# Performance work log

Hardware: AMD Instinct MI355X
Metric: run time of the kernel (lower is better)

Reference implementation:

```python
import jax, jax.numpy as jnp
import numpy as np
import math

NUM_GRIDS = 128
INPUT_DIM = 128
OUTPUT_DIM = 128
BATCH = 8192
INIT_SCALE = 0.1


def _borders_cdf_grid(n_chunks):
    # inverse Laplace CDF grid borders, exactly as in the torch module
    def inv(u):
        return np.log(2.0 * u) if u <= 0.5 else -np.log(2.0 * (1.0 - u))
    cs = 1.0 / n_chunks
    b = [inv(i * cs) for i in range(1, n_chunks)]
    left = b[0] - (b[1] - b[0])
    right = b[-1] + (b[-1] - b[-2])
    return np.array([left] + b + [right], dtype=np.float32)  # [n_chunks+1]


def setup_inputs() -> dict:
    key = jax.random.key(0)
    kx, kp = jax.random.split(key)
    x = jax.random.normal(kx, (INPUT_DIM, BATCH), dtype=jnp.float32)
    s = INIT_SCALE / math.sqrt(INPUT_DIM)
    func_parameter = jax.random.uniform(
        kp, (NUM_GRIDS + 1, OUTPUT_DIM, INPUT_DIM), dtype=jnp.float32,
        minval=-s, maxval=s)
    borders = jnp.asarray(_borders_cdf_grid(NUM_GRIDS))
    inverse_chunk_lengths = 1.0 / (borders[1:] - borders[:-1])  # [NUM_GRIDS]
    return {"x": x, "func_parameter": func_parameter,
            "borders": borders, "inverse_chunk_lengths": inverse_chunk_lengths}


def reference(x, func_parameter, borders, inverse_chunk_lengths):
    # x: [I, B]; func_parameter: [G+1, O, I]
    G = borders.shape[0] - 1
    I = x.shape[0]
    # Laplace CDF: R -> [0, 1]
    exp_na = jnp.exp(-jnp.abs(x))
    cdf = jnp.where(x > 0, 1.0 - 0.5 * exp_na, 0.5 * exp_na)
    # bucketize on uniform CDF grid (truncation == floor since cdf*G >= 0)
    idx = jnp.clip((cdf * G).astype(jnp.int32), 0, G - 1)        # [I, B]
    idx_next = jnp.clip(idx + 1, 0, G)                           # [I, B]
    left = borders[idx]                                          # [I, B]
    inv_len = inverse_chunk_lengths[idx]                         # [I, B]
    d = (x - left) * inv_len                                     # [I, B]
    # gather per-input-dim parameter rows: val[i, b, o] = P[idx[i,b], o, i]
    Pt = jnp.transpose(func_parameter, (2, 0, 1))                # [I, G+1, O]
    rows = jnp.arange(I)[:, None]                                # [I, 1]
    val_l = Pt[rows, idx]                                        # [I, B, O]
    val_r = Pt[rows, idx_next]                                   # [I, B, O]
    out = ((1.0 - d)[..., None] * val_l + d[..., None] * val_r).sum(axis=0)  # [B, O]
    return out.T                                                 # [O, B]
```

## Files before the change

kernel.cpp:

```cpp
#include <hip/hip_runtime.h>
#include <cstdint>


#define NG 128
#define NI 128
#define NO 128
#define NB 8192

using half2v  = __attribute__((ext_vector_type(2))) _Float16;
using float4v = __attribute__((ext_vector_type(4))) float;

__device__ inline uint32_t pack_f16x2(float lo, float hi) {
    _Float16 hl = (_Float16)lo, hh = (_Float16)hi;
    return (uint32_t)__builtin_bit_cast(unsigned short, hl) |
           ((uint32_t)__builtin_bit_cast(unsigned short, hh) << 16);
}

__device__ inline void load_lds16(const uint32_t* g, uint32_t* l) {
    __builtin_amdgcn_global_load_lds(
        (const __attribute__((address_space(1))) uint32_t*)g,
        (__attribute__((address_space(3))) uint32_t*)l, 16, 0, 0);
}

__global__ __launch_bounds__(256) void build_q(const float* __restrict__ P,
                                               uint32_t* __restrict__ Q2) {
    __shared__ float L[5][16][128];
    const int gb = blockIdx.x >> 3;
    const int ob = blockIdx.x & 7;
    const int g0 = gb * 4;
    const int o0 = ob * 16;
    const int s0 = ob * 4;
    const int t  = threadIdx.x;
    #pragma unroll
    for (int pass = 0; pass < 40; ++pass) {
        int row = pass * 2 + (t >> 7);
        int i   = t & 127;
        int gg  = row >> 4, ol = row & 15;
        L[gg][ol][i] = P[(size_t)(g0 + gg) * (NO * NI) + (o0 + ol) * NI + i];
    }
    __syncthreads();
    #pragma unroll
    for (int pp = 0; pp < 2; ++pp) {
        int item = pp * 256 + t;
        int i  = item & 127;
        int sl = item >> 7;
        uint32_t* dst = Q2 + ((size_t)((s0 + sl) * NI + i) * NG + g0) * 4;
        #pragma unroll
        for (int gg = 0; gg < 4; ++gg) {
            uint32_t r[4];
            #pragma unroll
            for (int ow = 0; ow < 4; ++ow) {
                float pl = L[gg][sl * 4 + ow][i];
                float dd = L[gg + 1][sl * 4 + ow][i] - pl;
                r[ow] = pack_f16x2(pl, dd);
            }
            *(uint4*)(dst + gg * 4) = make_uint4(r[0], r[1], r[2], r[3]);
        }
    }
}

__global__ __launch_bounds__(256) void build_t(const float* __restrict__ x,
                                               const float* __restrict__ borders,
                                               const float* __restrict__ icl,
                                               uint32_t* __restrict__ T) {
    const int e0 = (blockIdx.x * 256 + threadIdx.x) * 4;
    const float4 xv = *(const float4*)(x + e0);
    uint32_t r[4];
    const float xs[4] = {xv.x, xv.y, xv.z, xv.w};
    #pragma unroll
    for (int k = 0; k < 4; ++k) {
        float v = xs[k];
        float ea = __expf(-fabsf(v));
        float cdf = v > 0.f ? 1.f - 0.5f * ea : 0.5f * ea;
        int idx = (int)(cdf * 128.f);
        idx = idx > 127 ? 127 : idx;
        float d = (v - borders[idx]) * icl[idx];
        _Float16 hd = (_Float16)d;
        r[k] = ((uint32_t)idx << 4) |
               ((uint32_t)__builtin_bit_cast(unsigned short, hd) << 16);
    }
    *(uint4*)(T + e0) = make_uint4(r[0], r[1], r[2], r[3]);
}

__global__ __launch_bounds__(1024, 4) void main_k(const uint32_t* __restrict__ Q2,
                                                  const uint32_t* __restrict__ T,
                                                  float* __restrict__ part) {
    __shared__ __align__(16) uint32_t slab[64 * NG * 4];
    const int t   = threadIdx.x;
    const int bx  = blockIdx.x;
    const int win = bx & 7;
    const int s   = bx >> 3;
    const int ih  = win >> 2;
    const int bq  = win & 3;
    const uint32_t* Qs = Q2 + ((size_t)s * NI + ih * 64) * (NG * 4);

    #pragma unroll
    for (int k = 0; k < 8; ++k)
        load_lds16(Qs + (size_t)(t + k * 1024) * 4, &slab[(t + k * 1024) * 4]);
    __syncthreads();

    #pragma unroll
    for (int bb = 0; bb < 2; ++bb) {
        const int bcol = (bq << 11) + (bb << 10) + t;
        const uint32_t* Tb = T + (size_t)(ih * 64) * NB + bcol;
        float a0 = 0.f, a1 = 0.f, a2 = 0.f, a3 = 0.f;
        uint32_t tt[16];
        #pragma unroll
        for (int il = 0; il < 16; ++il)
            tt[il] = Tb[(size_t)il * NB];
        #pragma unroll
        for (int ic = 0; ic < 4; ++ic) {
            uint32_t tn[16];
            if (ic < 3) {
                #pragma unroll
                for (int il = 0; il < 16; ++il)
                    tn[il] = Tb[(size_t)((ic + 1) * 16 + il) * NB];
            }
            const char* sp = (const char*)slab + ic * 32768;
            #pragma unroll
            for (int il = 0; il < 16; ++il) {
                uint32_t tw  = tt[il];
                uint32_t off = tw & 0xFFFFu;
                uint32_t w2b = (tw & 0xFFFF0000u) | 0x3C00u;
                uint4 q = *(const uint4*)(sp + il * 2048 + off);
                half2v w2 = __builtin_bit_cast(half2v, w2b);
                a0 = __builtin_amdgcn_fdot2(__builtin_bit_cast(half2v, q.x), w2, a0, false);
                a1 = __builtin_amdgcn_fdot2(__builtin_bit_cast(half2v, q.y), w2, a1, false);
                a2 = __builtin_amdgcn_fdot2(__builtin_bit_cast(half2v, q.z), w2, a2, false);
                a3 = __builtin_amdgcn_fdot2(__builtin_bit_cast(half2v, q.w), w2, a3, false);
            }
            if (ic < 3) {
                #pragma unroll
                for (int il = 0; il < 16; ++il)
                    tt[il] = tn[il];
            }
        }
        float* po = part + (size_t)ih * (NO * NB) + (size_t)(s * 4) * NB + bcol;
        po[0]              = a0;
        po[NB]             = a1;
        po[2 * (size_t)NB] = a2;
        po[3 * (size_t)NB] = a3;
    }
}

__global__ __launch_bounds__(256) void reduce_k(const float* __restrict__ part,
                                                float* __restrict__ out) {
    const int e0 = (blockIdx.x * 256 + threadIdx.x) * 4;
    const float4v v0 = *(const float4v*)(part + e0);
    const float4v v1 = *(const float4v*)(part + (size_t)NO * NB + e0);
    const float4v r  = v0 + v1;
    __builtin_nontemporal_store(r, (float4v*)(out + e0));
}

extern "C" void kernel_launch(void* const* d_in, const int* in_sizes, int n_in,
                              void* d_out, int out_size, void* d_ws, size_t ws_size,
                              hipStream_t stream) {
    const float* x       = (const float*)d_in[0];
    const float* P       = (const float*)d_in[1];
    const float* borders = (const float*)d_in[2];
    const float* icl     = (const float*)d_in[3];
    float* out = (float*)d_out;

    uint32_t* Q2  = (uint32_t*)d_ws;
    uint32_t* T   = Q2 + (size_t)NO * NI * NG;
    float*    prt = (float*)(T + (size_t)NI * NB);

    hipLaunchKernelGGL(build_q, dim3(256), dim3(256), 0, stream, P, Q2);
    hipLaunchKernelGGL(build_t, dim3(NI * NB / 1024), dim3(256), 0, stream,
                       x, borders, icl, T);
    hipLaunchKernelGGL(main_k, dim3(256), dim3(1024), 0, stream, Q2, T, prt);
    hipLaunchKernelGGL(reduce_k, dim3(NO * NB / 1024), dim3(256), 0, stream,
                       prt, out);
}
```

Baseline: 108.6 us.

## Split main kernel into four input-dim quarters with 1024 blocks and smaller LDS slabs

The main kernel now assigns each block 32 input dims and one 1024-column batch tile instead of 64 input dims and two batch tiles. This quadruples the grid and halves the LDS slab, and the launch bound now requests higher occupancy, with block indices mapped so that batch tiles follow the XCD index. The first T loads are issued before the barrier so they overlap the LDS fill. In exchange the partial-sum buffer doubles to four slices, and the reduce kernel must read and add four partials instead of two, which adds global memory traffic.

```diff
diff --git a/kernel.cpp b/kernel.cpp
--- a/kernel.cpp
+++ b/kernel.cpp
@@ -82,73 +82,75 @@
     *(uint4*)(T + e0) = make_uint4(r[0], r[1], r[2], r[3]);
 }
 
-__global__ __launch_bounds__(1024, 4) void main_k(const uint32_t* __restrict__ Q2,
+__global__ __launch_bounds__(1024, 8) void main_k(const uint32_t* __restrict__ Q2,
                                                   const uint32_t* __restrict__ T,
                                                   float* __restrict__ part) {
-    __shared__ __align__(16) uint32_t slab[64 * NG * 4];
-    const int t   = threadIdx.x;
-    const int bx  = blockIdx.x;
-    const int win = bx & 7;
-    const int s   = bx >> 3;
-    const int ih  = win >> 2;
-    const int bq  = win & 3;
-    const uint32_t* Qs = Q2 + ((size_t)s * NI + ih * 64) * (NG * 4);
+    __shared__ __align__(16) uint32_t slab[32 * NG * 4];
+    const int t    = threadIdx.x;
+    const int bx   = blockIdx.x;
+    const int xcd  = bx & 7;
+    const int s    = (bx >> 3) & 31;
+    const int widx = bx >> 8;
+    const int iq   = ((widx << 3) | xcd) >> 3;
+    const int bt   = xcd;
+    const int bme  = (bt << 10) | t;
+    const uint32_t* Qs = Q2 + ((size_t)s * NI + iq * 32) * (NG * 4);
+    const uint32_t* Tb = T + (size_t)(iq * 32) * NB + bme;
 
     #pragma unroll
-    for (int k = 0; k < 8; ++k)
+    for (int k = 0; k < 4; ++k)
         load_lds16(Qs + (size_t)(t + k * 1024) * 4, &slab[(t + k * 1024) * 4]);
+    uint32_t tt[16];
+    #pragma unroll
+    for (int il = 0; il < 16; ++il)
+        tt[il] = Tb[(size_t)il * NB];
     __syncthreads();
 
+    float a0 = 0.f, a1 = 0.f, a2 = 0.f, a3 = 0.f;
     #pragma unroll
-    for (int bb = 0; bb < 2; ++bb) {
-        const int bcol = (bq << 11) + (bb << 10) + t;
-        const uint32_t* Tb = T + (size_t)(ih * 64) * NB + bcol;
-        float a0 = 0.f, a1 = 0.f, a2 = 0.f, a3 = 0.f;
-        uint32_t tt[16];
+    for (int ic = 0; ic < 2; ++ic) {
+        uint32_t tn[16];
+        if (ic == 0) {
+            #pragma unroll
+            for (int il = 0; il < 16; ++il)
+                tn[il] = Tb[(size_t)(16 + il) * NB];
+        }
+        const char* sp = (const char*)slab + ic * 32768;
         #pragma unroll
-        for (int il = 0; il < 16; ++il)
-            tt[il] = Tb[(size_t)il * NB];
-        #pragma unroll
-        for (int ic = 0; ic < 4; ++ic) {
-            uint32_t tn[16];
-            if (ic < 3) {
-                #pragma unroll
-                for (int il = 0; il < 16; ++il)
-                    tn[il] = Tb[(size_t)((ic + 1) * 16 + il) * NB];
-            }
-            const char* sp = (const char*)slab + ic * 32768;
+        for (int il = 0; il < 16; ++il) {
+            uint32_t tw  = tt[il];
+            uint32_t off = tw & 0xFFFFu;
+            uint32_t w2b = (tw & 0xFFFF0000u) | 0x3C00u;
+            uint4 q = *(const uint4*)(sp + il * 2048 + off);
+            half2v w2 = __builtin_bit_cast(half2v, w2b);
+            a0 = __builtin_amdgcn_fdot2(__builtin_bit_cast(half2v, q.x), w2, a0, false);
+            a1 = __builtin_amdgcn_fdot2(__builtin_bit_cast(half2v, q.y), w2, a1, false);
+            a2 = __builtin_amdgcn_fdot2(__builtin_bit_cast(half2v, q.z), w2, a2, false);
+            a3 = __builtin_amdgcn_fdot2(__builtin_bit_cast(half2v, q.w), w2, a3, false);
+        }
+        if (ic == 0) {
             #pragma unroll
-            for (int il = 0; il < 16; ++il) {
-                uint32_t tw  = tt[il];
-                uint32_t off = tw & 0xFFFFu;
-                uint32_t w2b = (tw & 0xFFFF0000u) | 0x3C00u;
-                uint4 q = *(const uint4*)(sp + il * 2048 + off);
-                half2v w2 = __builtin_bit_cast(half2v, w2b);
-                a0 = __builtin_amdgcn_fdot2(__builtin_bit_cast(half2v, q.x), w2, a0, false);
-                a1 = __builtin_amdgcn_fdot2(__builtin_bit_cast(half2v, q.y), w2, a1, false);
-                a2 = __builtin_amdgcn_fdot2(__builtin_bit_cast(half2v, q.z), w2, a2, false);
-                a3 = __builtin_amdgcn_fdot2(__builtin_bit_cast(half2v, q.w), w2, a3, false);
-            }
-            if (ic < 3) {
-                #pragma unroll
-                for (int il = 0; il < 16; ++il)
-                    tt[il] = tn[il];
-            }
+            for (int il = 0; il < 16; ++il)
+                tt[il] = tn[il];
         }
-        float* po = part + (size_t)ih * (NO * NB) + (size_t)(s * 4) * NB + bcol;
-        po[0]              = a0;
-        po[NB]             = a1;
-        po[2 * (size_t)NB] = a2;
-        po[3 * (size_t)NB] = a3;
     }
+
+    float* po = part + (size_t)iq * (NO * NB) + (size_t)(s * 4) * NB + bme;
+    po[0]              = a0;
+    po[NB]             = a1;
+    po[2 * (size_t)NB] = a2;
+    po[3 * (size_t)NB] = a3;
 }
 
 __global__ __launch_bounds__(256) void reduce_k(const float* __restrict__ part,
                                                 float* __restrict__ out) {
     const int e0 = (blockIdx.x * 256 + threadIdx.x) * 4;
+    const size_t st = (size_t)NO * NB;
     const float4v v0 = *(const float4v*)(part + e0);
-    const float4v v1 = *(const float4v*)(part + (size_t)NO * NB + e0);
-    const float4v r  = v0 + v1;
+    const float4v v1 = *(const float4v*)(part + st + e0);
+    const float4v v2 = *(const float4v*)(part + 2 * st + e0);
+    const float4v v3 = *(const float4v*)(part + 3 * st + e0);
+    const float4v r  = (v0 + v1) + (v2 + v3);
     __builtin_nontemporal_store(r, (float4v*)(out + e0));
 }
 
@@ -168,7 +170,7 @@
     hipLaunchKernelGGL(build_q, dim3(256), dim3(256), 0, stream, P, Q2);
     hipLaunchKernelGGL(build_t, dim3(NI * NB / 1024), dim3(256), 0, stream,
                        x, borders, icl, T);
-    hipLaunchKernelGGL(main_k, dim3(256), dim3(1024), 0, stream, Q2, T, prt);
+    hipLaunchKernelGGL(main_k, dim3(1024), dim3(1024), 0, stream, Q2, T, prt);
     hipLaunchKernelGGL(reduce_k, dim3(NO * NB / 1024), dim3(256), 0, stream,
                        prt, out);
 }
```

Result: faster. 105.0 us (-3.4%).
